# Kernel tuning notes

Hardware: AMD Instinct MI355X
Metric: run time of the kernel (lower is better)

Reference implementation:

```python
import jax, jax.numpy as jnp
import numpy as np
from jax import lax

ROUTINGS = 3
SCALING = 2
NUM_CAPSULE = 8
NUM_ATOMS = 16
EPS = 1e-9


def squash(v):
    # SegCaps squash: v * |v|^2 / ((1+|v|^2) * |v|), norm over last axis
    sq = jnp.sum(v * v, axis=-1, keepdims=True)
    return v * sq / ((1.0 + sq) * jnp.sqrt(sq + EPS))


def setup_inputs() -> dict:
    key = jax.random.key(0)
    k1, k2 = jax.random.split(key)
    B, H, Wd, Cin, Ain = 4, 56, 56, 8, 32
    x = jax.random.normal(k1, (B, H, Wd, Cin, Ain), dtype=jnp.float32)
    # TF conv2d_transpose filter layout: [k, k, out_ch, in_ch]
    W = jax.random.normal(k2, (4, 4, NUM_CAPSULE * NUM_ATOMS, Ain), dtype=jnp.float32) * 0.05
    b = 0.1 * jnp.ones((1, 1, NUM_CAPSULE, NUM_ATOMS), dtype=jnp.float32)
    return {"x": x, "W": W, "b": b}


def reference(x, W, b):
    B, H, Wd, Cin, Ain = x.shape
    Cout, Aout = NUM_CAPSULE, NUM_ATOMS
    # [B,H,W,Cin,A] -> [Cin,B,H,W,A] -> [Cin*B,H,W,A]  (faithful to original ordering)
    xt = jnp.transpose(x, (3, 0, 1, 2, 4)).reshape(Cin * B, H, Wd, Ain)
    # TF conv2d_transpose, SAME padding, stride=scaling: out spatial = in * scaling
    out = lax.conv_transpose(
        xt, W, strides=(SCALING, SCALING), padding="SAME",
        dimension_numbers=("NHWC", "HWIO", "NHWC"), transpose_kernel=True)
    Hp, Wp = out.shape[1], out.shape[2]
    # votes: [B, Cin, Hp, Wp, Cout, Aout]  (faithful to original reshape)
    votes = out.reshape(B, Cin, Hp, Wp, Cout, Aout)
    biases = jnp.broadcast_to(b, (Hp, Wp, Cout, Aout))
    logits = jnp.zeros((B, Cin, Hp, Wp, Cout), dtype=x.dtype)
    act = None
    for i in range(ROUTINGS):
        route = jax.nn.softmax(logits, axis=-1)                      # [B,Cin,Hp,Wp,Cout]
        pre = jnp.einsum("bihwc,bihwca->bhwca", route, votes) + biases
        act = squash(pre)                                            # [B,Hp,Wp,Cout,Aout]
        if i < ROUTINGS - 1:
            logits = logits + jnp.einsum("bihwca,bhwca->bihwc", votes, act)
    return act
```

## Files before the change

### kernel.cpp

```cpp
#include <hip/hip_runtime.h>
#include <math.h>

#define CEPS 1e-9f

typedef _Float16 half8 __attribute__((ext_vector_type(8)));
typedef _Float16 h2 __attribute__((ext_vector_type(2)));
typedef __fp16 fp16x2 __attribute__((ext_vector_type(2)));
typedef float floatx16 __attribute__((ext_vector_type(16)));
typedef float f32x4v __attribute__((ext_vector_type(4)));


template<int CTRL>
__device__ __forceinline__ float dpp_add(float v) {
    return v + __int_as_float(__builtin_amdgcn_update_dpp(
        0, __float_as_int(v), CTRL, 0xF, 0xF, false));
}
template<int CTRL>
__device__ __forceinline__ h2 dpp_add_h2(h2 v) {
    int t = __builtin_amdgcn_update_dpp(
        0, __builtin_bit_cast(int, v), CTRL, 0xF, 0xF, false);
    return v + __builtin_bit_cast(h2, t);
}
__device__ __forceinline__ h2 sum_i8_h2(h2 v) {
    v = dpp_add_h2<0xB1>(v);
    v = dpp_add_h2<0x4E>(v);
    v = dpp_add_h2<0x141>(v);
    return v;
}
__device__ __forceinline__ h2 pkrtz(float a, float b) {
    return __builtin_bit_cast(h2, __builtin_amdgcn_cvt_pkrtz(a, b));
}
__device__ __forceinline__ float fdot2(h2 a, h2 b, float c) {
    return __builtin_amdgcn_fdot2(__builtin_bit_cast(fp16x2, a),
                                  __builtin_bit_cast(fp16x2, b), c, false);
}
__device__ __forceinline__ h2 hsel(bool c, h2 a, h2 b) {
    int r = c ? __builtin_bit_cast(int, a) : __builtin_bit_cast(int, b);
    return __builtin_bit_cast(h2, r);
}

__global__ __launch_bounds__(256) void prep_w(const float* __restrict__ Wt,
                                              _Float16* __restrict__ wb) {
    int idx = blockIdx.x * 256 + threadIdx.x;
    int parity = idx >> 11;
    int s = (idx >> 8) & 7;
    int t = (idx >> 6) & 3;
    int l = idx & 63;
    int rh = parity >> 1, rw = parity & 1;
    int n = t * 32 + (l & 31);
    int h = l >> 5;
    int ci0 = ((s & 1) << 4) + (h << 3);
    int kh = ((s >> 2) << 1) + 1 - rh;
    int kw = (((s >> 1) & 1) << 1) + 1 - rw;
    const float* src = Wt + (((kh * 4 + kw) * 128 + n) << 5) + ci0;
    float4 w0 = *(const float4*)src;
    float4 w1 = *(const float4*)(src + 4);
    half8 hv;
    hv[0] = (_Float16)w0.x; hv[1] = (_Float16)w0.y;
    hv[2] = (_Float16)w0.z; hv[3] = (_Float16)w0.w;
    hv[4] = (_Float16)w1.x; hv[5] = (_Float16)w1.y;
    hv[6] = (_Float16)w1.z; hv[7] = (_Float16)w1.w;
    *(half8*)(wb + ((long)idx << 3)) = hv;
}

__global__ __launch_bounds__(256, 4) void caps_mfma(
    const float* __restrict__ x,
    const _Float16* __restrict__ wb,
    const float* __restrict__ bias,
    float* __restrict__ out)
{
    __shared__ _Float16 xt[25 * 8 * 40];
    __shared__ float scx[4][1056];

    const int tid = threadIdx.x;
    const int tile = blockIdx.x;
    const int tu = tile / 14, tv = tile - tu * 14;
    const int u0 = tu * 4, v0 = tv * 4;
    const int rh = blockIdx.y >> 1;
    const int rw = blockIdx.y & 1;
    const int bp = blockIdx.z;
    const _Float16* wsrc = wb + ((long)blockIdx.y << 14);

    #pragma unroll
    for (int it = 0; it < 4; ++it) {
        int idx = tid + (it << 8);
        if (idx < 800) {
            int cell = idx >> 5;
            int r = idx & 31;
            int i = r >> 2;
            int ci0 = (r & 3) << 3;
            int ri = cell / 5, rj = cell - ri * 5;
            int gi = u0 + rh - 1 + ri;
            int gj = v0 + rw - 1 + rj;
            float tmp[8] = {0.f, 0.f, 0.f, 0.f, 0.f, 0.f, 0.f, 0.f};
            if ((unsigned)gi < 56u && (unsigned)gj < 56u) {
                const float* src = x + (((i & 3) * 56 + gi) * 56 + gj) * 256
                                     + ((bp * 2 + (i >> 2)) << 5) + ci0;
                float4 a0 = *(const float4*)src;
                float4 a1 = *(const float4*)(src + 4);
                tmp[0] = a0.x; tmp[1] = a0.y; tmp[2] = a0.z; tmp[3] = a0.w;
                tmp[4] = a1.x; tmp[5] = a1.y; tmp[6] = a1.z; tmp[7] = a1.w;
            }
            half8 hv;
            #pragma unroll
            for (int j = 0; j < 8; ++j) hv[j] = (_Float16)tmp[j];
            *(half8*)(xt + (cell * 8 + i) * 40 + ci0) = hv;
        }
    }
    __syncthreads();

    const int l = tid & 63;
    const int w = tid >> 6;
    const int col = l & 31, h = l >> 5;
    const int invA = (l & 31) * 40 + (h << 3);

    floatx16 acc[4];
    #pragma unroll
    for (int t = 0; t < 4; ++t)
        #pragma unroll
        for (int j = 0; j < 16; ++j) acc[t][j] = 0.f;

    #pragma unroll
    for (int s = 0; s < 8; ++s) {
        const int tkh = s >> 2;
        const int tkw = (s >> 1) & 1;
        const int row = w + 1 - tkh;
        const int aoff = (row * 5 + 1 - tkw) * 320 + ((s & 1) << 4) + invA;
        half8 af = *(const half8*)(xt + aoff);
        #pragma unroll
        for (int t = 0; t < 4; ++t) {
            half8 bf = *(const half8*)(wsrc + (((s * 4 + t) * 64 + l) << 3));
            acc[t] = __builtin_amdgcn_mfma_f32_32x32x16_f16(af, bf, acc[t], 0, 0, 0);
        }
    }

    float* scb = &scx[w][0];
    const int cI = l >> 3;
    const int iI = l & 7;

    h2 bq2[8];
    {
        const float* bpt = bias + (cI << 4);
        float4 b0 = *(const float4*)bpt;
        float4 b1 = *(const float4*)(bpt + 4);
        float4 b2 = *(const float4*)(bpt + 8);
        float4 b3 = *(const float4*)(bpt + 12);
        bq2[0] = pkrtz(b0.x, b0.y); bq2[1] = pkrtz(b0.z, b0.w);
        bq2[2] = pkrtz(b1.x, b1.y); bq2[3] = pkrtz(b1.z, b1.w);
        bq2[4] = pkrtz(b2.x, b2.y); bq2[5] = pkrtz(b2.z, b2.w);
        bq2[6] = pkrtz(b3.x, b3.y); bq2[7] = pkrtz(b3.z, b3.w);
    }
    const h2 c0125 = pkrtz(0.125f, 0.125f);

    #pragma unroll
    for (int pixl = 0; pixl < 4; ++pixl) {
        #pragma unroll
        for (int t = 0; t < 4; ++t)
            #pragma unroll
            for (int il = 0; il < 4; ++il)
                scb[((h << 2) + il) * 132 + t * 32 + col] = acc[t][pixl * 4 + il];

        const float* rb = scb + iI * 132 + (cI << 4);
        f32x4v vq0 = *(const f32x4v*)(rb);
        f32x4v vq1 = *(const f32x4v*)(rb + 4);
        f32x4v vq2 = *(const f32x4v*)(rb + 8);
        f32x4v vq3 = *(const f32x4v*)(rb + 12);
        h2 va2[8];
        va2[0] = pkrtz(vq0.x, vq0.y); va2[1] = pkrtz(vq0.z, vq0.w);
        va2[2] = pkrtz(vq1.x, vq1.y); va2[3] = pkrtz(vq1.z, vq1.w);
        va2[4] = pkrtz(vq2.x, vq2.y); va2[5] = pkrtz(vq2.z, vq2.w);
        va2[6] = pkrtz(vq3.x, vq3.y); va2[7] = pkrtz(vq3.z, vq3.w);

        h2 pre2[8];
        float lg;

        #pragma unroll
        for (int j = 0; j < 8; ++j) {
            h2 s2 = sum_i8_h2(va2[j]);
            pre2[j] = s2 * c0125 + bq2[j];
        }
        {
            float nq = fdot2(pre2[0], pre2[0], 0.f);
            #pragma unroll
            for (int j = 1; j < 8; ++j) nq = fdot2(pre2[j], pre2[j], nq);
            float sc = nq * __builtin_amdgcn_rcpf(1.f + nq)
                          * __builtin_amdgcn_rsqf(nq + CEPS);
            h2 sc2 = pkrtz(sc, sc);
            #pragma unroll
            for (int j = 0; j < 8; ++j) pre2[j] *= sc2;
            float d = fdot2(va2[0], pre2[0], 0.f);
            #pragma unroll
            for (int j = 1; j < 8; ++j) d = fdot2(va2[j], pre2[j], d);
            lg = d;
        }

        #pragma unroll
        for (int r = 1; r < 3; ++r) {
            float e = __expf(lg);
            float ss = dpp_add<0x128>(e);
            ss += __int_as_float(__builtin_amdgcn_ds_swizzle(
                      __float_as_int(ss), 0x401F));
            ss += __shfl_xor(ss, 32);
            float route = e * __builtin_amdgcn_rcpf(ss);
            h2 rt2 = pkrtz(route, route);
            #pragma unroll
            for (int j = 0; j < 8; ++j) {
                h2 p = sum_i8_h2(rt2 * va2[j]);
                pre2[j] = p + bq2[j];
            }
            float nq = fdot2(pre2[0], pre2[0], 0.f);
            #pragma unroll
            for (int j = 1; j < 8; ++j) nq = fdot2(pre2[j], pre2[j], nq);
            float sc = nq * __builtin_amdgcn_rcpf(1.f + nq)
                          * __builtin_amdgcn_rsqf(nq + CEPS);
            h2 sc2 = pkrtz(sc, sc);
            #pragma unroll
            for (int j = 0; j < 8; ++j) pre2[j] *= sc2;
            if (r < 2) {
                float d = lg;
                #pragma unroll
                for (int j = 0; j < 8; ++j) d = fdot2(va2[j], pre2[j], d);
                lg = d;
            }
        }

        if (iI < 4) {
            h2 h0 = hsel((iI & 2) != 0, pre2[4], pre2[0]);
            h2 h1 = hsel((iI & 2) != 0, pre2[5], pre2[1]);
            h2 h2_ = hsel((iI & 2) != 0, pre2[6], pre2[2]);
            h2 h3 = hsel((iI & 2) != 0, pre2[7], pre2[3]);
            h2 p0 = hsel((iI & 1) != 0, h2_, h0);
            h2 p1 = hsel((iI & 1) != 0, h3, h1);
            float4 o4 = make_float4((float)p0.x, (float)p0.y,
                                    (float)p1.x, (float)p1.y);
            const int p = ((u0 + w) << 1) + rh;
            const int q = ((v0 + pixl) << 1) + rw;
            *(float4*)(out + (((bp * 112 + p) * 112 + q) << 7) + cI * 16 + iI * 4) = o4;
        }
    }
}

extern "C" void kernel_launch(void* const* d_in, const int* in_sizes, int n_in,
                              void* d_out, int out_size, void* d_ws, size_t ws_size,
                              hipStream_t stream) {
    const float* x  = (const float*)d_in[0];
    const float* Wt = (const float*)d_in[1];
    const float* b  = (const float*)d_in[2];
    float* out = (float*)d_out;
    _Float16* wb = (_Float16*)d_ws;

    prep_w<<<32, 256, 0, stream>>>(Wt, wb);
    dim3 grid(196, 4, 4);
    caps_mfma<<<grid, 256, 0, stream>>>(x, wb, b, out);
}
```

Baseline: 116.7 us.

## Raise occupancy: pack accumulators to fp16, alias LDS buffers, split dot chains

The kernel now targets 6 waves per SIMD instead of 4. To fit, the MFMA work is split into two halves with two accumulators each, and results are packed to fp16 pairs, which reduces live accumulator registers. The x tile and scratch LDS buffers are aliased into one region behind an extra barrier, which cuts LDS per block. The serial fdot2 reduction chains are split into four independent partial sums to shorten dependency latency. The cost is extra fp16 rounding of the votes before the scratch stage and a possible risk of register spills under the tighter bound.

After: 350.5 us. +200.4%, slower.

```diff
diff --git a/kernel.cpp b/kernel.cpp
--- a/kernel.cpp
+++ b/kernel.cpp
@@ -63,14 +63,15 @@
     *(half8*)(wb + ((long)idx << 3)) = hv;
 }
 
-__global__ __launch_bounds__(256, 4) void caps_mfma(
+__global__ __launch_bounds__(256, 6) void caps_mfma(
     const float* __restrict__ x,
     const _Float16* __restrict__ wb,
     const float* __restrict__ bias,
     float* __restrict__ out)
 {
-    __shared__ _Float16 xt[25 * 8 * 40];
-    __shared__ float scx[4][1056];
+    __shared__ __align__(16) unsigned char smem[4 * 1056 * 4];
+    _Float16* xt = (_Float16*)smem;
+    float (*scx)[1056] = (float (*)[1056])smem;
 
     const int tid = threadIdx.x;
     const int tile = blockIdx.x;
@@ -114,25 +115,33 @@
     const int col = l & 31, h = l >> 5;
     const int invA = (l & 31) * 40 + (h << 3);
 
-    floatx16 acc[4];
+    h2 pf[4][8];
     #pragma unroll
-    for (int t = 0; t < 4; ++t)
-        #pragma unroll
-        for (int j = 0; j < 16; ++j) acc[t][j] = 0.f;
-
-    #pragma unroll
-    for (int s = 0; s < 8; ++s) {
-        const int tkh = s >> 2;
-        const int tkw = (s >> 1) & 1;
-        const int row = w + 1 - tkh;
-        const int aoff = (row * 5 + 1 - tkw) * 320 + ((s & 1) << 4) + invA;
-        half8 af = *(const half8*)(xt + aoff);
-        #pragma unroll
-        for (int t = 0; t < 4; ++t) {
-            half8 bf = *(const half8*)(wsrc + (((s * 4 + t) * 64 + l) << 3));
-            acc[t] = __builtin_amdgcn_mfma_f32_32x32x16_f16(af, bf, acc[t], 0, 0, 0);
-        }
-    }
+    for (int half = 0; half < 2; ++half) {
+        floatx16 acc0, acc1;
+        #pragma unroll
+        for (int j = 0; j < 16; ++j) { acc0[j] = 0.f; acc1[j] = 0.f; }
+        const int tb = half << 1;
+        #pragma unroll
+        for (int s = 0; s < 8; ++s) {
+            const int tkh = s >> 2;
+            const int tkw = (s >> 1) & 1;
+            const int row = w + 1 - tkh;
+            const int aoff = (row * 5 + 1 - tkw) * 320 + ((s & 1) << 4) + invA;
+            half8 af = *(const half8*)(xt + aoff);
+            half8 bf0 = *(const half8*)(wsrc + (((s * 4 + tb) * 64 + l) << 3));
+            half8 bf1 = *(const half8*)(wsrc + (((s * 4 + tb + 1) * 64 + l) << 3));
+            acc0 = __builtin_amdgcn_mfma_f32_32x32x16_f16(af, bf0, acc0, 0, 0, 0);
+            acc1 = __builtin_amdgcn_mfma_f32_32x32x16_f16(af, bf1, acc1, 0, 0, 0);
+        }
+        #pragma unroll
+        for (int m = 0; m < 8; ++m) {
+            pf[tb][m]     = pkrtz(acc0[2 * m], acc0[2 * m + 1]);
+            pf[tb + 1][m] = pkrtz(acc1[2 * m], acc1[2 * m + 1]);
+        }
+    }
+
+    __syncthreads();
 
     float* scb = &scx[w][0];
     const int cI = l >> 3;
@@ -157,8 +166,11 @@
         #pragma unroll
         for (int t = 0; t < 4; ++t)
             #pragma unroll
-            for (int il = 0; il < 4; ++il)
-                scb[((h << 2) + il) * 132 + t * 32 + col] = acc[t][pixl * 4 + il];
+            for (int il = 0; il < 4; ++il) {
+                h2 pp = pf[t][(pixl << 1) + (il >> 1)];
+                float v = (il & 1) ? (float)pp.y : (float)pp.x;
+                scb[((h << 2) + il) * 132 + t * 32 + col] = v;
+            }
 
         const float* rb = scb + iI * 132 + (cI << 4);
         f32x4v vq0 = *(const f32x4v*)(rb);
@@ -180,18 +192,29 @@
             pre2[j] = s2 * c0125 + bq2[j];
         }
         {
-            float nq = fdot2(pre2[0], pre2[0], 0.f);
-            #pragma unroll
-            for (int j = 1; j < 8; ++j) nq = fdot2(pre2[j], pre2[j], nq);
+            float n0 = fdot2(pre2[0], pre2[0], 0.f);
+            float n1 = fdot2(pre2[1], pre2[1], 0.f);
+            float n2 = fdot2(pre2[2], pre2[2], 0.f);
+            float n3 = fdot2(pre2[3], pre2[3], 0.f);
+            n0 = fdot2(pre2[4], pre2[4], n0);
+            n1 = fdot2(pre2[5], pre2[5], n1);
+            n2 = fdot2(pre2[6], pre2[6], n2);
+            n3 = fdot2(pre2[7], pre2[7], n3);
+            float nq = (n0 + n1) + (n2 + n3);
             float sc = nq * __builtin_amdgcn_rcpf(1.f + nq)
                           * __builtin_amdgcn_rsqf(nq + CEPS);
             h2 sc2 = pkrtz(sc, sc);
             #pragma unroll
             for (int j = 0; j < 8; ++j) pre2[j] *= sc2;
-            float d = fdot2(va2[0], pre2[0], 0.f);
-            #pragma unroll
-            for (int j = 1; j < 8; ++j) d = fdot2(va2[j], pre2[j], d);
-            lg = d;
+            float d0 = fdot2(va2[0], pre2[0], 0.f);
+            float d1 = fdot2(va2[1], pre2[1], 0.f);
+            float d2 = fdot2(va2[2], pre2[2], 0.f);
+            float d3 = fdot2(va2[3], pre2[3], 0.f);
+            d0 = fdot2(va2[4], pre2[4], d0);
+            d1 = fdot2(va2[5], pre2[5], d1);
+            d2 = fdot2(va2[6], pre2[6], d2);
+            d3 = fdot2(va2[7], pre2[7], d3);
+            lg = (d0 + d1) + (d2 + d3);
         }
 
         #pragma unroll
@@ -208,19 +231,30 @@
                 h2 p = sum_i8_h2(rt2 * va2[j]);
                 pre2[j] = p + bq2[j];
             }
-            float nq = fdot2(pre2[0], pre2[0], 0.f);
-            #pragma unroll
-            for (int j = 1; j < 8; ++j) nq = fdot2(pre2[j], pre2[j], nq);
+            float n0 = fdot2(pre2[0], pre2[0], 0.f);
+            float n1 = fdot2(pre2[1], pre2[1], 0.f);
+            float n2 = fdot2(pre2[2], pre2[2], 0.f);
+            float n3 = fdot2(pre2[3], pre2[3], 0.f);
+            n0 = fdot2(pre2[4], pre2[4], n0);
+            n1 = fdot2(pre2[5], pre2[5], n1);
+            n2 = fdot2(pre2[6], pre2[6], n2);
+            n3 = fdot2(pre2[7], pre2[7], n3);
+            float nq = (n0 + n1) + (n2 + n3);
             float sc = nq * __builtin_amdgcn_rcpf(1.f + nq)
                           * __builtin_amdgcn_rsqf(nq + CEPS);
             h2 sc2 = pkrtz(sc, sc);
             #pragma unroll
             for (int j = 0; j < 8; ++j) pre2[j] *= sc2;
             if (r < 2) {
-                float d = lg;
-                #pragma unroll
-                for (int j = 0; j < 8; ++j) d = fdot2(va2[j], pre2[j], d);
-                lg = d;
+                float d0 = fdot2(va2[0], pre2[0], lg);
+                float d1 = fdot2(va2[1], pre2[1], 0.f);
+                float d2 = fdot2(va2[2], pre2[2], 0.f);
+                float d3 = fdot2(va2[3], pre2[3], 0.f);
+                d0 = fdot2(va2[4], pre2[4], d0);
+                d1 = fdot2(va2[5], pre2[5], d1);
+                d2 = fdot2(va2[6], pre2[6], d2);
+                d3 = fdot2(va2[7], pre2[7], d3);
+                lg = (d0 + d1) + (d2 + d3);
             }
         }
 
```
